# Kernel tuning notes

Hardware: AMD Instinct MI355X
Metric: run time of the kernel (lower is better)

Reference implementation:

```python
import jax, jax.numpy as jnp
import numpy as np

B, S, DIM, H = 8, 1024, 1024, 16
D = DIM // H  # d_head = 64


def setup_inputs() -> dict:
    key = jax.random.key(0)
    ks = jax.random.split(key, 7)
    scale = 1.0 / np.sqrt(D)  # nn.Linear default init range ~ U(-1/sqrt(in), 1/sqrt(in))
    x = jax.random.normal(ks[0], (B, S, DIM), dtype=jnp.float32)
    Wq = jax.random.uniform(ks[1], (H, D, D), jnp.float32, -scale, scale)
    Wk = jax.random.uniform(ks[2], (H, D, D), jnp.float32, -scale, scale)
    Wv = jax.random.uniform(ks[3], (H, D, D), jnp.float32, -scale, scale)
    bq = jax.random.uniform(ks[4], (H, D), jnp.float32, -scale, scale)
    bk = jax.random.uniform(ks[5], (H, D), jnp.float32, -scale, scale)
    bv = jax.random.uniform(ks[6], (H, D), jnp.float32, -scale, scale)
    return {"x": x, "Wq": Wq, "Wk": Wk, "Wv": Wv, "bq": bq, "bk": bk, "bv": bv}


def reference(x, Wq, Wk, Wv, bq, bk, bv):
    # x: [B,S,DIM] -> split heads: [B,S,H,D] (matches per-head column slicing)
    xh = x.reshape(x.shape[0], x.shape[1], H, D)
    # per-head linear: y = x @ W.T + b  (nn.Linear convention: weight [out,in])
    q = jnp.einsum('bshd,hed->bshe', xh, Wq) + bq  # [B,S,H,D]
    k = jnp.einsum('bshd,hed->bshe', xh, Wk) + bk
    v = jnp.einsum('bshd,hed->bshe', xh, Wv) + bv
    scores = jnp.einsum('bqhd,bkhd->bhqk', q, k) / jnp.sqrt(jnp.float32(D))
    attn = jax.nn.softmax(scores, axis=-1)  # [B,H,S,S]
    out = jnp.einsum('bhqk,bkhd->bqhd', attn, v)  # [B,S,H,D]
    # hstack over heads == merge last two dims back to DIM
    return out.reshape(x.shape[0], x.shape[1], H * D)
```

## Files before the change

### kernel.cpp

```cpp
#include <hip/hip_runtime.h>
#include <hip/hip_bf16.h>

#define BB 8
#define SS 1024
#define HH 16
#define DD 64
#define DIMM 1024
#define NUNITS (BB * HH)
#define UNIT_ELEMS (SS * DD)

typedef __attribute__((ext_vector_type(8))) short short8;
typedef __attribute__((ext_vector_type(4))) float f32x4;

#if __has_builtin(__builtin_amdgcn_exp2f)
#define EXP2F(x) __builtin_amdgcn_exp2f(x)
#else
#define EXP2F(x) exp2f(x)
#endif
#if __has_builtin(__builtin_amdgcn_rcpf)
#define RCPF(x) __builtin_amdgcn_rcpf(x)
#else
#define RCPF(x) (1.0f / (x))
#endif

__device__ inline short f2b(float f) {
    unsigned u = __float_as_uint(f);
    u = (u + 0x7FFFu + ((u >> 16) & 1u)) >> 16;
    return (short)u;
}
__device__ inline unsigned pk2(float lo, float hi) {
    unsigned a = __float_as_uint(lo), b = __float_as_uint(hi);
    a = (a + 0x7FFFu + ((a >> 16) & 1u)) >> 16;
    b = (b + 0x7FFFu + ((b >> 16) & 1u)) & 0xFFFF0000u;
    return a | b;
}

__global__ __launch_bounds__(256) void qkv_proj(
    const float* __restrict__ x, const float* __restrict__ Wq,
    const float* __restrict__ Wk, const float* __restrict__ Wv,
    const float* __restrict__ bqp, const float* __restrict__ bkp,
    const float* __restrict__ bvp,
    short* __restrict__ Qo, short* __restrict__ Ko, short* __restrict__ Vto,
    int unit0)
{
    __shared__ alignas(16) short wsm[3][64][72];
    __shared__ alignas(16) short xs[64][72];
    __shared__ alignas(16) short tr[64][72];

    const int t = threadIdx.x;
    const int bid = blockIdx.x;
    const int stg = bid & 3;
    const int ul = bid >> 2;
    const int unit = unit0 + ul;
    const int h = unit & 15;
    const int b = unit >> 4;

    for (int m = 0; m < 3; ++m) {
        const float* src = ((m == 0) ? Wq : (m == 1) ? Wk : Wv) + h * DD * DD;
        for (int i = 0; i < 4; ++i) {
            int g = t + i * 256;
            int e = g >> 4, c = (g & 15) * 4;
            float4 wv = *reinterpret_cast<const float4*>(src + e * DD + c);
            short4 sv; sv.x = f2b(wv.x); sv.y = f2b(wv.y); sv.z = f2b(wv.z); sv.w = f2b(wv.w);
            *reinterpret_cast<short4*>(&wsm[m][e][c]) = sv;
        }
    }

    const int lane = t & 63, w = t >> 6;
    const int l15 = lane & 15, quad = lane >> 4;

    for (int st2 = 0; st2 < 4; ++st2) {
        const int s0 = (stg * 4 + st2) * 64;
        if (st2) __syncthreads();
        for (int i = 0; i < 4; ++i) {
            int g = t + i * 256;
            int r = g >> 4, c = (g & 15) * 4;
            float4 xv = *reinterpret_cast<const float4*>(
                x + ((size_t)(b * SS + s0 + r)) * DIMM + h * DD + c);
            short4 sv; sv.x = f2b(xv.x); sv.y = f2b(xv.y); sv.z = f2b(xv.z); sv.w = f2b(xv.w);
            *reinterpret_cast<short4*>(&xs[r][c]) = sv;
        }
        __syncthreads();

        short8 a0 = *reinterpret_cast<const short8*>(&xs[w * 16 + l15][quad * 8]);
        short8 a1 = *reinterpret_cast<const short8*>(&xs[w * 16 + l15][32 + quad * 8]);

        f32x4 acc[12];
        for (int m = 0; m < 3; ++m)
            for (int et = 0; et < 4; ++et) {
                short8 w0 = *reinterpret_cast<const short8*>(&wsm[m][et * 16 + l15][quad * 8]);
                short8 w1 = *reinterpret_cast<const short8*>(&wsm[m][et * 16 + l15][32 + quad * 8]);
                f32x4 a = {0.f, 0.f, 0.f, 0.f};
                a = __builtin_amdgcn_mfma_f32_16x16x32_bf16(a0, w0, a, 0, 0, 0);
                a = __builtin_amdgcn_mfma_f32_16x16x32_bf16(a1, w1, a, 0, 0, 0);
                acc[m * 4 + et] = a;
            }

        for (int m = 0; m < 3; ++m) {
            if (m) __syncthreads();
            const float* bp = (m == 0) ? bqp : (m == 1) ? bkp : bvp;
            const float scale = (m == 0) ? 0.125f : 1.0f;
            for (int et = 0; et < 4; ++et) {
                float bias = bp[h * DD + et * 16 + l15];
                int e = et * 16 + l15;
                for (int r = 0; r < 4; ++r) {
                    float v = (acc[m * 4 + et][r] + bias) * scale;
                    int srow = w * 16 + quad * 4 + r;
                    if (m == 2) tr[e][srow] = f2b(v);
                    else        tr[srow][e] = f2b(v);
                }
            }
            __syncthreads();
            for (int i = 0; i < 2; ++i) {
                int g = t + i * 256;
                int row = g >> 3, col = (g & 7) * 8;
                short8 val = *reinterpret_cast<const short8*>(&tr[row][col]);
                if (m == 0)
                    *reinterpret_cast<short8*>(Qo + ((size_t)ul * SS + s0 + row) * DD + col) = val;
                else if (m == 1)
                    *reinterpret_cast<short8*>(Ko + ((size_t)ul * SS + s0 + row) * DD + col) = val;
                else
                    *reinterpret_cast<short8*>(Vto + ((size_t)ul * DD + row) * SS + s0 + col) = val;
            }
        }
    }
}

__global__ __launch_bounds__(256, 4) void attn(
    const short* __restrict__ Q, const short* __restrict__ K,
    const short* __restrict__ Vt, float* __restrict__ out, int unit0, int nu)
{
    __shared__ alignas(16) short ks[64][72];
    __shared__ alignas(16) short vts[64][72];
    __shared__ alignas(16) short ps[4][32][72];

    const int t = threadIdx.x;
    const int bid = blockIdx.x;
    int ul, qt;
    if (nu == NUNITS) {
        int xslot = bid & 7;
        int j = bid >> 3;
        ul = xslot * 16 + (j & 15);
        qt = j >> 4;
    } else {
        ul = bid >> 3;
        qt = bid & 7;
    }
    const int unit = unit0 + ul;
    const int h = unit & 15;
    const int b = unit >> 4;
    const int q0 = qt * 128;
    const int lane = t & 63, w = t >> 6;
    const int l15 = lane & 15, quad = lane >> 4;

    short8 qa[2][2];
    for (int s = 0; s < 2; ++s) {
        const short* qp = Q + ((size_t)ul * SS + q0 + s * 64 + w * 16 + l15) * DD;
        qa[s][0] = *reinterpret_cast<const short8*>(qp + quad * 8);
        qa[s][1] = *reinterpret_cast<const short8*>(qp + 32 + quad * 8);
    }

    short8 ones;
    for (int j = 0; j < 8; ++j) ones[j] = (short)0x3F80;

    f32x4 o[8];
    f32x4 lacc[2];
    for (int i = 0; i < 8; ++i) o[i] = (f32x4){0.f, 0.f, 0.f, 0.f};
    lacc[0] = (f32x4){0.f, 0.f, 0.f, 0.f};
    lacc[1] = (f32x4){0.f, 0.f, 0.f, 0.f};

    const int srow_ = t >> 3, scol = (t & 7) * 8;

    const short* kg = K + (size_t)ul * UNIT_ELEMS + srow_ * DD + scol;
    const short* vg = Vt + (size_t)ul * UNIT_ELEMS + srow_ * SS + scol;
    char* ksw = (char*)&ks[srow_][scol];
    char* vtw = (char*)&vts[srow_][scol];
    const char* kbp = (const char*)&ks[l15][quad * 8];
    const char* vbp = (const char*)&vts[l15][quad * 8];
    const char* pap = (const char*)&ps[w][l15][quad * 8];
    char* psw = (char*)&ps[w][l15][quad * 4];

    const float L2E = 1.44269504f;
    const float MBIAS = 11.5415603f;

    for (int kt = 0; kt < 16; ++kt) {
        __syncthreads();
        *reinterpret_cast<short8*>(ksw) = *reinterpret_cast<const short8*>(kg);
        *reinterpret_cast<short8*>(ksw + 32 * 144) = *reinterpret_cast<const short8*>(kg + 32 * DD);
        *reinterpret_cast<short8*>(vtw) = *reinterpret_cast<const short8*>(vg);
        *reinterpret_cast<short8*>(vtw + 32 * 144) = *reinterpret_cast<const short8*>(vg + 32 * SS);
        kg += 64 * DD;
        vg += 64;
        __syncthreads();

        for (int n = 0; n < 4; ++n) {
            short8 kb0 = *reinterpret_cast<const short8*>(kbp + n * 2304);
            short8 kb1 = *reinterpret_cast<const short8*>(kbp + n * 2304 + 64);
            for (int s = 0; s < 2; ++s) {
                f32x4 a = {0.f, 0.f, 0.f, 0.f};
                a = __builtin_amdgcn_mfma_f32_16x16x32_bf16(kb0, qa[s][0], a, 0, 0, 0);
                a = __builtin_amdgcn_mfma_f32_16x16x32_bf16(kb1, qa[s][1], a, 0, 0, 0);
                float p0 = EXP2F(fmaf(a[0], L2E, -MBIAS));
                float p1 = EXP2F(fmaf(a[1], L2E, -MBIAS));
                float p2 = EXP2F(fmaf(a[2], L2E, -MBIAS));
                float p3 = EXP2F(fmaf(a[3], L2E, -MBIAS));
                uint2 pk; pk.x = pk2(p0, p1); pk.y = pk2(p2, p3);
                *reinterpret_cast<uint2*>(psw + s * 2304 + n * 32) = pk;
            }
        }

        short8 pa[2][2];
        for (int s = 0; s < 2; ++s) {
            pa[s][0] = *reinterpret_cast<const short8*>(pap + s * 2304);
            pa[s][1] = *reinterpret_cast<const short8*>(pap + s * 2304 + 64);
            lacc[s] = __builtin_amdgcn_mfma_f32_16x16x32_bf16(pa[s][0], ones, lacc[s], 0, 0, 0);
            lacc[s] = __builtin_amdgcn_mfma_f32_16x16x32_bf16(pa[s][1], ones, lacc[s], 0, 0, 0);
        }
        for (int dt = 0; dt < 4; ++dt) {
            short8 vb0 = *reinterpret_cast<const short8*>(vbp + dt * 2304);
            short8 vb1 = *reinterpret_cast<const short8*>(vbp + dt * 2304 + 64);
            for (int s = 0; s < 2; ++s) {
                o[s * 4 + dt] = __builtin_amdgcn_mfma_f32_16x16x32_bf16(pa[s][0], vb0, o[s * 4 + dt], 0, 0, 0);
                o[s * 4 + dt] = __builtin_amdgcn_mfma_f32_16x16x32_bf16(pa[s][1], vb1, o[s * 4 + dt], 0, 0, 0);
            }
        }
    }

    float* outp = out + ((size_t)b * SS + q0 + w * 16 + quad * 4) * DIMM + h * DD + l15;
    for (int s = 0; s < 2; ++s)
        for (int r = 0; r < 4; ++r) {
            float rin = RCPF(lacc[s][r]);
            for (int dt = 0; dt < 4; ++dt)
                outp[(size_t)(s * 64 + r) * DIMM + dt * 16] = o[s * 4 + dt][r] * rin;
        }
}

extern "C" void kernel_launch(void* const* d_in, const int* in_sizes, int n_in,
                              void* d_out, int out_size, void* d_ws, size_t ws_size,
                              hipStream_t stream) {
    const float* x   = (const float*)d_in[0];
    const float* Wq  = (const float*)d_in[1];
    const float* Wk  = (const float*)d_in[2];
    const float* Wv  = (const float*)d_in[3];
    const float* bqp = (const float*)d_in[4];
    const float* bkp = (const float*)d_in[5];
    const float* bvp = (const float*)d_in[6];
    float* out = (float*)d_out;

    const size_t unit_bytes = 3ULL * UNIT_ELEMS * sizeof(short);
    int U = (int)(ws_size / unit_bytes);
    if (U < 1) U = 1;
    if (U > NUNITS) U = NUNITS;

    short* Qw  = (short*)d_ws;
    short* Kw  = Qw + (size_t)U * UNIT_ELEMS;
    short* Vtw = Kw + (size_t)U * UNIT_ELEMS;

    for (int u0 = 0; u0 < NUNITS; u0 += U) {
        int nu = NUNITS - u0 < U ? NUNITS - u0 : U;
        qkv_proj<<<dim3(nu * 4), dim3(256), 0, stream>>>(
            x, Wq, Wk, Wv, bqp, bkp, bvp, Qw, Kw, Vtw, u0);
        attn<<<dim3(nu * 8), dim3(256), 0, stream>>>(Qw, Kw, Vtw, out, u0, nu);
    }
}
```

Measured before the change: 152.6 us.

## Drop K bias, fold V bias into output, keep weights in registers

```diff
diff --git a/kernel.cpp b/kernel.cpp
--- a/kernel.cpp
+++ b/kernel.cpp
@@ -34,18 +34,24 @@
     b = (b + 0x7FFFu + ((b >> 16) & 1u)) & 0xFFFF0000u;
     return a | b;
 }
+__device__ inline short8 pack8(float4 a, float4 b) {
+    short8 o;
+    o[0] = f2b(a.x); o[1] = f2b(a.y); o[2] = f2b(a.z); o[3] = f2b(a.w);
+    o[4] = f2b(b.x); o[5] = f2b(b.y); o[6] = f2b(b.z); o[7] = f2b(b.w);
+    return o;
+}
 
 __global__ __launch_bounds__(256) void qkv_proj(
     const float* __restrict__ x, const float* __restrict__ Wq,
     const float* __restrict__ Wk, const float* __restrict__ Wv,
-    const float* __restrict__ bqp, const float* __restrict__ bkp,
-    const float* __restrict__ bvp,
+    const float* __restrict__ bqp,
     short* __restrict__ Qo, short* __restrict__ Ko, short* __restrict__ Vto,
     int unit0)
 {
-    __shared__ alignas(16) short wsm[3][64][72];
     __shared__ alignas(16) short xs[64][72];
-    __shared__ alignas(16) short tr[64][72];
+    __shared__ alignas(16) short qtm[64][72];
+    __shared__ alignas(16) short ktm[64][72];
+    __shared__ alignas(16) short vtm[64][72];
 
     const int t = threadIdx.x;
     const int bid = blockIdx.x;
@@ -55,19 +61,23 @@
     const int h = unit & 15;
     const int b = unit >> 4;
 
-    for (int m = 0; m < 3; ++m) {
-        const float* src = ((m == 0) ? Wq : (m == 1) ? Wk : Wv) + h * DD * DD;
-        for (int i = 0; i < 4; ++i) {
-            int g = t + i * 256;
-            int e = g >> 4, c = (g & 15) * 4;
-            float4 wv = *reinterpret_cast<const float4*>(src + e * DD + c);
-            short4 sv; sv.x = f2b(wv.x); sv.y = f2b(wv.y); sv.z = f2b(wv.z); sv.w = f2b(wv.w);
-            *reinterpret_cast<short4*>(&wsm[m][e][c]) = sv;
-        }
-    }
-
     const int lane = t & 63, w = t >> 6;
     const int l15 = lane & 15, quad = lane >> 4;
+
+    short8 wq[4][2], wk[4][2], wv[4][2];
+    {
+        const size_t wb = (size_t)h * DD * DD + (size_t)l15 * DD + quad * 8;
+        for (int et = 0; et < 4; ++et)
+            for (int c = 0; c < 2; ++c) {
+                size_t off = wb + (size_t)et * 16 * DD + c * 32;
+                wq[et][c] = pack8(*reinterpret_cast<const float4*>(Wq + off),
+                                  *reinterpret_cast<const float4*>(Wq + off + 4));
+                wk[et][c] = pack8(*reinterpret_cast<const float4*>(Wk + off),
+                                  *reinterpret_cast<const float4*>(Wk + off + 4));
+                wv[et][c] = pack8(*reinterpret_cast<const float4*>(Wv + off),
+                                  *reinterpret_cast<const float4*>(Wv + off + 4));
+            }
+    }
 
     for (int st2 = 0; st2 < 4; ++st2) {
         const int s0 = (stg * 4 + st2) * 64;
@@ -82,53 +92,48 @@
         }
         __syncthreads();
 
-        short8 a0 = *reinterpret_cast<const short8*>(&xs[w * 16 + l15][quad * 8]);
-        short8 a1 = *reinterpret_cast<const short8*>(&xs[w * 16 + l15][32 + quad * 8]);
-
-        f32x4 acc[12];
-        for (int m = 0; m < 3; ++m)
-            for (int et = 0; et < 4; ++et) {
-                short8 w0 = *reinterpret_cast<const short8*>(&wsm[m][et * 16 + l15][quad * 8]);
-                short8 w1 = *reinterpret_cast<const short8*>(&wsm[m][et * 16 + l15][32 + quad * 8]);
-                f32x4 a = {0.f, 0.f, 0.f, 0.f};
-                a = __builtin_amdgcn_mfma_f32_16x16x32_bf16(a0, w0, a, 0, 0, 0);
-                a = __builtin_amdgcn_mfma_f32_16x16x32_bf16(a1, w1, a, 0, 0, 0);
-                acc[m * 4 + et] = a;
-            }
-
-        for (int m = 0; m < 3; ++m) {
-            if (m) __syncthreads();
-            const float* bp = (m == 0) ? bqp : (m == 1) ? bkp : bvp;
-            const float scale = (m == 0) ? 0.125f : 1.0f;
-            for (int et = 0; et < 4; ++et) {
-                float bias = bp[h * DD + et * 16 + l15];
-                int e = et * 16 + l15;
-                for (int r = 0; r < 4; ++r) {
-                    float v = (acc[m * 4 + et][r] + bias) * scale;
-                    int srow = w * 16 + quad * 4 + r;
-                    if (m == 2) tr[e][srow] = f2b(v);
-                    else        tr[srow][e] = f2b(v);
-                }
-            }
-            __syncthreads();
-            for (int i = 0; i < 2; ++i) {
-                int g = t + i * 256;
-                int row = g >> 3, col = (g & 7) * 8;
-                short8 val = *reinterpret_cast<const short8*>(&tr[row][col]);
-                if (m == 0)
-                    *reinterpret_cast<short8*>(Qo + ((size_t)ul * SS + s0 + row) * DD + col) = val;
-                else if (m == 1)
-                    *reinterpret_cast<short8*>(Ko + ((size_t)ul * SS + s0 + row) * DD + col) = val;
-                else
-                    *reinterpret_cast<short8*>(Vto + ((size_t)ul * DD + row) * SS + s0 + col) = val;
-            }
+        short8 xa0 = *reinterpret_cast<const short8*>(&xs[w * 16 + l15][quad * 8]);
+        short8 xa1 = *reinterpret_cast<const short8*>(&xs[w * 16 + l15][32 + quad * 8]);
+
+        for (int et = 0; et < 4; ++et) {
+            f32x4 aq = {0.f, 0.f, 0.f, 0.f};
+            aq = __builtin_amdgcn_mfma_f32_16x16x32_bf16(wq[et][0], xa0, aq, 0, 0, 0);
+            aq = __builtin_amdgcn_mfma_f32_16x16x32_bf16(wq[et][1], xa1, aq, 0, 0, 0);
+            f32x4 ak = {0.f, 0.f, 0.f, 0.f};
+            ak = __builtin_amdgcn_mfma_f32_16x16x32_bf16(wk[et][0], xa0, ak, 0, 0, 0);
+            ak = __builtin_amdgcn_mfma_f32_16x16x32_bf16(wk[et][1], xa1, ak, 0, 0, 0);
+            f32x4 av = {0.f, 0.f, 0.f, 0.f};
+            av = __builtin_amdgcn_mfma_f32_16x16x32_bf16(xa0, wv[et][0], av, 0, 0, 0);
+            av = __builtin_amdgcn_mfma_f32_16x16x32_bf16(xa1, wv[et][1], av, 0, 0, 0);
+
+            float4 bq4 = *reinterpret_cast<const float4*>(bqp + h * DD + et * 16 + quad * 4);
+            uint2 pq;
+            pq.x = pk2((aq[0] + bq4.x) * 0.125f, (aq[1] + bq4.y) * 0.125f);
+            pq.y = pk2((aq[2] + bq4.z) * 0.125f, (aq[3] + bq4.w) * 0.125f);
+            *reinterpret_cast<uint2*>(&qtm[w * 16 + l15][et * 16 + quad * 4]) = pq;
+            uint2 pkk; pkk.x = pk2(ak[0], ak[1]); pkk.y = pk2(ak[2], ak[3]);
+            *reinterpret_cast<uint2*>(&ktm[w * 16 + l15][et * 16 + quad * 4]) = pkk;
+            uint2 pv; pv.x = pk2(av[0], av[1]); pv.y = pk2(av[2], av[3]);
+            *reinterpret_cast<uint2*>(&vtm[et * 16 + l15][w * 16 + quad * 4]) = pv;
+        }
+        __syncthreads();
+        for (int i = 0; i < 2; ++i) {
+            int g = t + i * 256;
+            int row = g >> 3, col = (g & 7) * 8;
+            *reinterpret_cast<short8*>(Qo + ((size_t)ul * SS + s0 + row) * DD + col) =
+                *reinterpret_cast<const short8*>(&qtm[row][col]);
+            *reinterpret_cast<short8*>(Ko + ((size_t)ul * SS + s0 + row) * DD + col) =
+                *reinterpret_cast<const short8*>(&ktm[row][col]);
+            *reinterpret_cast<short8*>(Vto + ((size_t)ul * DD + row) * SS + s0 + col) =
+                *reinterpret_cast<const short8*>(&vtm[row][col]);
         }
     }
 }
 
 __global__ __launch_bounds__(256, 4) void attn(
     const short* __restrict__ Q, const short* __restrict__ K,
-    const short* __restrict__ Vt, float* __restrict__ out, int unit0, int nu)
+    const short* __restrict__ Vt, const float* __restrict__ bvp,
+    float* __restrict__ out, int unit0, int nu)
 {
     __shared__ alignas(16) short ks[64][72];
     __shared__ alignas(16) short vts[64][72];
@@ -226,12 +231,14 @@
         }
     }
 
+    float bvv[4];
+    for (int dt = 0; dt < 4; ++dt) bvv[dt] = bvp[h * DD + dt * 16 + l15];
     float* outp = out + ((size_t)b * SS + q0 + w * 16 + quad * 4) * DIMM + h * DD + l15;
     for (int s = 0; s < 2; ++s)
         for (int r = 0; r < 4; ++r) {
             float rin = RCPF(lacc[s][r]);
             for (int dt = 0; dt < 4; ++dt)
-                outp[(size_t)(s * 64 + r) * DIMM + dt * 16] = o[s * 4 + dt][r] * rin;
+                outp[(size_t)(s * 64 + r) * DIMM + dt * 16] = fmaf(o[s * 4 + dt][r], rin, bvv[dt]);
         }
 }
 
@@ -243,7 +250,6 @@
     const float* Wk  = (const float*)d_in[2];
     const float* Wv  = (const float*)d_in[3];
     const float* bqp = (const float*)d_in[4];
-    const float* bkp = (const float*)d_in[5];
     const float* bvp = (const float*)d_in[6];
     float* out = (float*)d_out;
 
@@ -259,7 +265,7 @@
     for (int u0 = 0; u0 < NUNITS; u0 += U) {
         int nu = NUNITS - u0 < U ? NUNITS - u0 : U;
         qkv_proj<<<dim3(nu * 4), dim3(256), 0, stream>>>(
-            x, Wq, Wk, Wv, bqp, bkp, bvp, Qw, Kw, Vtw, u0);
-        attn<<<dim3(nu * 8), dim3(256), 0, stream>>>(Qw, Kw, Vtw, out, u0, nu);
-    }
-}
+            x, Wq, Wk, Wv, bqp, Qw, Kw, Vtw, u0);
+        attn<<<dim3(nu * 8), dim3(256), 0, stream>>>(Qw, Kw, Vtw, bvp, out, u0, nu);
+    }
+}
```

Result: slower. 159.8 us (+4.7%).
